# Optimization experiments

Measured on AMD Instinct MI355X. Metric: run time of the kernel, lower is better.

Reference implementation:

```python
import jax, jax.numpy as jnp
import numpy as np

PATCH = 16
LOSS_WEIGHT = 1.0


def setup_inputs() -> dict:
    key = jax.random.key(0)
    cls_score = jax.random.normal(key, (8, 19, 512, 512), dtype=jnp.float32)
    return {"cls_score": cls_score}


def reference(cls_score):
    # Faithful to NuclearLoss(patch_size=16, use_softmax=True, inverse=False,
    # reduction='mean').
    N, C, H, W = cls_score.shape
    p = PATCH
    ph, pw = H // p, W // p
    logits = jax.nn.softmax(cls_score, axis=1)  # softmax over channel dim
    # patchify: (N,C,H,W) -> (N*L, p*p, C) with L = ph*pw
    x = logits.reshape(N, C, ph, p, pw, p)
    x = jnp.einsum('nchpwq->nhwpqc', x)
    patches = x.reshape(N * ph * pw, p * p, C)  # (B, p^2, C)
    # Original: mats = sqrt(bmm(P^T, P)) elementwise, loss = -sum(trace(mat)).
    # Only the diagonal of P^T P is needed: diag_k = sum_i P[i,k]^2.
    diag = jnp.sum(patches * patches, axis=1)          # (B, C)
    loss = -jnp.sum(jnp.sqrt(diag))
    loss = loss / patches.shape[0]                      # reduction='mean'
    return LOSS_WEIGHT * loss
```

## Files before the change

kernel.cpp:

```cpp
#include <hip/hip_runtime.h>
#include <math.h>


#define NIMG 8
#define CCH  19
#define HH   512
#define WW   512
#define CHST (HH * WW)

__global__ __launch_bounds__(256, 4) void nuclear_loss_kernel(
    const float* __restrict__ in, float* __restrict__ out) {
    __shared__ float psum[4 * CCH];

    const int tid = threadIdx.x;
    const int b   = blockIdx.x;
    const int n    = b >> 8;
    const int rem  = b & 255;
    const int prow = rem >> 3;
    const int creg = rem & 7;
    const int col  = (creg << 6) + (tid & 63);
    const int row0 = (prow << 4) + (tid >> 6);
    const int plocal = (tid & 63) >> 4;

    for (int i = tid; i < 4 * CCH; i += 256) psum[i] = 0.0f;
    __syncthreads();

    float part[CCH];
#pragma unroll
    for (int c = 0; c < CCH; ++c) part[c] = 0.0f;

    const float* base = in + (size_t)n * CCH * CHST + (size_t)row0 * WW + col;

#pragma unroll
    for (int i = 0; i < 4; ++i) {
        const float* p = base + (size_t)(i * 4) * WW;
        float e[CCH];
        float s = 0.0f;
#pragma unroll
        for (int c = 0; c < CCH; ++c) {
            e[c] = __expf(p[(size_t)c * CHST]);
            s += e[c];
        }
        const float inv = 1.0f / s;
#pragma unroll
        for (int c = 0; c < CCH; ++c) {
            const float t = e[c] * inv;
            part[c] = fmaf(t, t, part[c]);
        }
    }

#pragma unroll
    for (int c = 0; c < CCH; ++c) {
        float v = part[c];
        v += __shfl_down(v, 8, 16);
        v += __shfl_down(v, 4, 16);
        v += __shfl_down(v, 2, 16);
        v += __shfl_down(v, 1, 16);
        part[c] = v;
    }

    if ((tid & 15) == 0) {
#pragma unroll
        for (int c = 0; c < CCH; ++c)
            atomicAdd(&psum[plocal * CCH + c], part[c]);
    }
    __syncthreads();

    if (tid < 64) {
        float v = (tid < 4 * CCH) ? sqrtf(psum[tid]) : 0.0f;
        if (tid + 64 < 4 * CCH) v += sqrtf(psum[tid + 64]);
        v += __shfl_down(v, 32, 64);
        v += __shfl_down(v, 16, 64);
        v += __shfl_down(v, 8, 64);
        v += __shfl_down(v, 4, 64);
        v += __shfl_down(v, 2, 64);
        v += __shfl_down(v, 1, 64);
        if (tid == 0) atomicAdd(out, v * (-1.0f / 8192.0f));
    }
}

extern "C" void kernel_launch(void* const* d_in, const int* in_sizes, int n_in,
                              void* d_out, int out_size, void* d_ws, size_t ws_size,
                              hipStream_t stream) {
    const float* in = (const float*)d_in[0];
    float* out = (float*)d_out;
    hipMemsetAsync(out, 0, sizeof(float), stream);
    nuclear_loss_kernel<<<2048, 256, 0, stream>>>(in, out);
}
```

Measured before the change: 223.7 us.

## Stage image rows into LDS via global_load_lds and reduce patches through global atomics

The kernel now has one block per image row. It copies all 19 channels of the row into LDS with direct global-to-LDS 16-byte loads, and each thread then computes the softmax for two adjacent pixels. Per-patch channel sums are reduced across 8 lanes and accumulated into a workspace with global atomics. A second kernel takes the square roots and reduces to the scalar. The goal is wider, better-coalesced loads and more memory-level parallelism, at the cost of many more global atomics (16 rows contend per patch entry), an extra memset and an extra launch, plus about 38 KB of LDS per block, which limits occupancy.

```diff
diff --git a/kernel.cpp b/kernel.cpp
--- a/kernel.cpp
+++ b/kernel.cpp
@@ -2,80 +2,103 @@
 #include <math.h>
 
 
-#define NIMG 8
-#define CCH  19
-#define HH   512
-#define WW   512
-#define CHST (HH * WW)
+#define CCH   19
+#define WW    512
+#define CHST  (512 * 512)
+#define IMGST (CCH * CHST)
+#define NPATCH 8192
 
-__global__ __launch_bounds__(256, 4) void nuclear_loss_kernel(
-    const float* __restrict__ in, float* __restrict__ out) {
-    __shared__ float psum[4 * CCH];
+typedef float f2 __attribute__((ext_vector_type(2)));
 
-    const int tid = threadIdx.x;
-    const int b   = blockIdx.x;
-    const int n    = b >> 8;
-    const int rem  = b & 255;
-    const int prow = rem >> 3;
-    const int creg = rem & 7;
-    const int col  = (creg << 6) + (tid & 63);
-    const int row0 = (prow << 4) + (tid >> 6);
-    const int plocal = (tid & 63) >> 4;
+__global__ __launch_bounds__(256, 4) void nuclear_patch_kernel(
+    const float* __restrict__ in, float* __restrict__ ws) {
+    __shared__ float lds[CCH * WW];
 
-    for (int i = tid; i < 4 * CCH; i += 256) psum[i] = 0.0f;
+    const int tid  = threadIdx.x;
+    const int w    = tid >> 6;
+    const int lane = tid & 63;
+    const int b    = blockIdx.x;
+    const int n    = b >> 9;
+    const int row  = b & 511;
+
+    const float* grow = in + (size_t)n * IMGST + (size_t)row * WW;
+    for (int j = 0; j < 10; ++j) {
+        const int i = w + j * 4;
+        if (i < 2 * CCH) {
+            const int ch   = i >> 1;
+            const int half = i & 1;
+            const float* g = grow + (size_t)ch * CHST + half * 256 + lane * 4;
+            const float* l = &lds[ch * WW + half * 256];
+            __builtin_amdgcn_global_load_lds(
+                (const __attribute__((address_space(1))) unsigned int*)g,
+                (__attribute__((address_space(3))) unsigned int*)l,
+                16, 0, 0);
+        }
+    }
     __syncthreads();
+
+    const f2* ldsv = (const f2*)lds;
+    f2 e[CCH];
+    f2 s2 = {0.0f, 0.0f};
+#pragma unroll
+    for (int c = 0; c < CCH; ++c) {
+        f2 x = ldsv[c * 256 + tid];
+        f2 ev;
+        ev.x = __expf(x.x);
+        ev.y = __expf(x.y);
+        e[c] = ev;
+        s2 += ev;
+    }
+    const float ix = 1.0f / s2.x;
+    const float iy = 1.0f / s2.y;
 
     float part[CCH];
 #pragma unroll
-    for (int c = 0; c < CCH; ++c) part[c] = 0.0f;
-
-    const float* base = in + (size_t)n * CCH * CHST + (size_t)row0 * WW + col;
-
-#pragma unroll
-    for (int i = 0; i < 4; ++i) {
-        const float* p = base + (size_t)(i * 4) * WW;
-        float e[CCH];
-        float s = 0.0f;
-#pragma unroll
-        for (int c = 0; c < CCH; ++c) {
-            e[c] = __expf(p[(size_t)c * CHST]);
-            s += e[c];
-        }
-        const float inv = 1.0f / s;
-#pragma unroll
-        for (int c = 0; c < CCH; ++c) {
-            const float t = e[c] * inv;
-            part[c] = fmaf(t, t, part[c]);
-        }
+    for (int c = 0; c < CCH; ++c) {
+        const float px = e[c].x * ix;
+        const float py = e[c].y * iy;
+        part[c] = px * px + py * py;
     }
 
 #pragma unroll
     for (int c = 0; c < CCH; ++c) {
         float v = part[c];
-        v += __shfl_down(v, 8, 16);
-        v += __shfl_down(v, 4, 16);
-        v += __shfl_down(v, 2, 16);
-        v += __shfl_down(v, 1, 16);
+        v += __shfl_down(v, 4, 8);
+        v += __shfl_down(v, 2, 8);
+        v += __shfl_down(v, 1, 8);
         part[c] = v;
     }
 
-    if ((tid & 15) == 0) {
+    if ((lane & 7) == 0) {
+        const int pcol = tid >> 3;
+        const int pr   = row >> 4;
+        float* wsp = ws + ((size_t)((n * 32 + pr) * 32 + pcol)) * CCH;
 #pragma unroll
-        for (int c = 0; c < CCH; ++c)
-            atomicAdd(&psum[plocal * CCH + c], part[c]);
+        for (int c = 0; c < CCH; ++c) atomicAdd(&wsp[c], part[c]);
     }
+}
+
+__global__ __launch_bounds__(256) void nuclear_finish_kernel(
+    const float* __restrict__ ws, float* __restrict__ out) {
+    const int pid = blockIdx.x * 256 + threadIdx.x;
+    const float* p = ws + (size_t)pid * CCH;
+    float s = 0.0f;
+#pragma unroll
+    for (int c = 0; c < CCH; ++c) s += sqrtf(p[c]);
+
+    s += __shfl_down(s, 32, 64);
+    s += __shfl_down(s, 16, 64);
+    s += __shfl_down(s, 8, 64);
+    s += __shfl_down(s, 4, 64);
+    s += __shfl_down(s, 2, 64);
+    s += __shfl_down(s, 1, 64);
+
+    __shared__ float wsum[4];
+    if ((threadIdx.x & 63) == 0) wsum[threadIdx.x >> 6] = s;
     __syncthreads();
-
-    if (tid < 64) {
-        float v = (tid < 4 * CCH) ? sqrtf(psum[tid]) : 0.0f;
-        if (tid + 64 < 4 * CCH) v += sqrtf(psum[tid + 64]);
-        v += __shfl_down(v, 32, 64);
-        v += __shfl_down(v, 16, 64);
-        v += __shfl_down(v, 8, 64);
-        v += __shfl_down(v, 4, 64);
-        v += __shfl_down(v, 2, 64);
-        v += __shfl_down(v, 1, 64);
-        if (tid == 0) atomicAdd(out, v * (-1.0f / 8192.0f));
+    if (threadIdx.x == 0) {
+        const float t = wsum[0] + wsum[1] + wsum[2] + wsum[3];
+        atomicAdd(out, t * (-1.0f / 8192.0f));
     }
 }
 
@@ -83,7 +106,12 @@
                               void* d_out, int out_size, void* d_ws, size_t ws_size,
                               hipStream_t stream) {
     const float* in = (const float*)d_in[0];
+    float* ws  = (float*)d_ws;
     float* out = (float*)d_out;
+
+    hipMemsetAsync(ws, 0, (size_t)NPATCH * CCH * sizeof(float), stream);
     hipMemsetAsync(out, 0, sizeof(float), stream);
-    nuclear_loss_kernel<<<2048, 256, 0, stream>>>(in, out);
+
+    nuclear_patch_kernel<<<4096, 256, 0, stream>>>(in, ws);
+    nuclear_finish_kernel<<<NPATCH / 256, 256, 0, stream>>>(ws, out);
 }
```

Result: slower. 330.5 us (+47.8%).

## Process full patch-row slabs per block with vectorized two-pass softmax loads

Applied to the files above, without the earlier changes.

Each 1024-thread block now covers a 16-row slab (one patch row) of an image, and every thread handles 8 contiguous pixels through float4 loads. Softmax is computed in two passes, with the second pass re-reading the input from global memory, so HBM or cache traffic for the input roughly doubles. In exchange it avoids holding 19 exponentials per pixel in registers. Per-patch partials are reduced through plain LDS stores instead of shared-memory atomics, and only one global atomic is issued per block. The grid shrinks from 2048 to 256 blocks, which may underfill the GPU's many CUs.

```diff
diff --git a/kernel.cpp b/kernel.cpp
--- a/kernel.cpp
+++ b/kernel.cpp
@@ -2,80 +2,98 @@
 #include <math.h>
 
 
-#define NIMG 8
-#define CCH  19
-#define HH   512
-#define WW   512
-#define CHST (HH * WW)
+#define CCH   19
+#define CHST  (512 * 512)
+#define IMGST (CCH * CHST)
 
-__global__ __launch_bounds__(256, 4) void nuclear_loss_kernel(
+typedef float f4 __attribute__((ext_vector_type(4)));
+
+__global__ __launch_bounds__(1024, 4) void nuclear_slab_kernel(
     const float* __restrict__ in, float* __restrict__ out) {
-    __shared__ float psum[4 * CCH];
+    __shared__ float psum[16 * 32 * CCH];
+    __shared__ float wsum[16];
 
-    const int tid = threadIdx.x;
-    const int b   = blockIdx.x;
-    const int n    = b >> 8;
-    const int rem  = b & 255;
-    const int prow = rem >> 3;
-    const int creg = rem & 7;
-    const int col  = (creg << 6) + (tid & 63);
-    const int row0 = (prow << 4) + (tid >> 6);
-    const int plocal = (tid & 63) >> 4;
+    const int tid  = threadIdx.x;
+    const int w    = tid >> 6;
+    const int lane = tid & 63;
+    const int b    = blockIdx.x;
+    const int n    = b >> 5;
+    const int prow = b & 31;
 
-    for (int i = tid; i < 4 * CCH; i += 256) psum[i] = 0.0f;
-    __syncthreads();
+    const float* base = in + (size_t)n * IMGST + (size_t)prow * 8192
+                           + (size_t)tid * 8;
+
+    f4 sA = {0.0f, 0.0f, 0.0f, 0.0f};
+    f4 sB = {0.0f, 0.0f, 0.0f, 0.0f};
+#pragma unroll
+    for (int c = 0; c < CCH; ++c) {
+        const f4* p = (const f4*)(base + (size_t)c * CHST);
+        const f4 xa = p[0];
+        const f4 xb = p[1];
+        f4 ea, eb;
+        ea.x = __expf(xa.x); ea.y = __expf(xa.y);
+        ea.z = __expf(xa.z); ea.w = __expf(xa.w);
+        eb.x = __expf(xb.x); eb.y = __expf(xb.y);
+        eb.z = __expf(xb.z); eb.w = __expf(xb.w);
+        sA += ea;
+        sB += eb;
+    }
+    f4 iA, iB;
+    iA.x = 1.0f / sA.x; iA.y = 1.0f / sA.y;
+    iA.z = 1.0f / sA.z; iA.w = 1.0f / sA.w;
+    iB.x = 1.0f / sB.x; iB.y = 1.0f / sB.y;
+    iB.z = 1.0f / sB.z; iB.w = 1.0f / sB.w;
 
     float part[CCH];
 #pragma unroll
     for (int c = 0; c < CCH; ++c) part[c] = 0.0f;
 
-    const float* base = in + (size_t)n * CCH * CHST + (size_t)row0 * WW + col;
-
 #pragma unroll
-    for (int i = 0; i < 4; ++i) {
-        const float* p = base + (size_t)(i * 4) * WW;
-        float e[CCH];
-        float s = 0.0f;
-#pragma unroll
-        for (int c = 0; c < CCH; ++c) {
-            e[c] = __expf(p[(size_t)c * CHST]);
-            s += e[c];
-        }
-        const float inv = 1.0f / s;
-#pragma unroll
-        for (int c = 0; c < CCH; ++c) {
-            const float t = e[c] * inv;
-            part[c] = fmaf(t, t, part[c]);
-        }
+    for (int c = 0; c < CCH; ++c) {
+        const f4* p = (const f4*)(base + (size_t)c * CHST);
+        const f4 xa = p[0];
+        const f4 xb = p[1];
+        f4 ea, eb;
+        ea.x = __expf(xa.x); ea.y = __expf(xa.y);
+        ea.z = __expf(xa.z); ea.w = __expf(xa.w);
+        eb.x = __expf(xb.x); eb.y = __expf(xb.y);
+        eb.z = __expf(xb.z); eb.w = __expf(xb.w);
+        const f4 pa = ea * iA;
+        const f4 pb = eb * iB;
+        float v = pa.x * pa.x + pa.y * pa.y + pa.z * pa.z + pa.w * pa.w
+                + pb.x * pb.x + pb.y * pb.y + pb.z * pb.z + pb.w * pb.w;
+        v += __shfl_down(v, 1, 2);
+        part[c] += v;
     }
 
+    if ((lane & 1) == 0) {
+        const int pc = lane >> 1;
+        float* dst = &psum[(w * 32 + pc) * CCH];
 #pragma unroll
-    for (int c = 0; c < CCH; ++c) {
-        float v = part[c];
-        v += __shfl_down(v, 8, 16);
-        v += __shfl_down(v, 4, 16);
-        v += __shfl_down(v, 2, 16);
-        v += __shfl_down(v, 1, 16);
-        part[c] = v;
-    }
-
-    if ((tid & 15) == 0) {
-#pragma unroll
-        for (int c = 0; c < CCH; ++c)
-            atomicAdd(&psum[plocal * CCH + c], part[c]);
+        for (int c = 0; c < CCH; ++c) dst[c] = part[c];
     }
     __syncthreads();
 
-    if (tid < 64) {
-        float v = (tid < 4 * CCH) ? sqrtf(psum[tid]) : 0.0f;
-        if (tid + 64 < 4 * CCH) v += sqrtf(psum[tid + 64]);
-        v += __shfl_down(v, 32, 64);
-        v += __shfl_down(v, 16, 64);
-        v += __shfl_down(v, 8, 64);
-        v += __shfl_down(v, 4, 64);
-        v += __shfl_down(v, 2, 64);
-        v += __shfl_down(v, 1, 64);
-        if (tid == 0) atomicAdd(out, v * (-1.0f / 8192.0f));
+    float v = 0.0f;
+    if (tid < 32 * CCH) {
+        float d = 0.0f;
+#pragma unroll
+        for (int r = 0; r < 16; ++r) d += psum[r * (32 * CCH) + tid];
+        v = sqrtf(d);
+    }
+    v += __shfl_down(v, 32, 64);
+    v += __shfl_down(v, 16, 64);
+    v += __shfl_down(v, 8, 64);
+    v += __shfl_down(v, 4, 64);
+    v += __shfl_down(v, 2, 64);
+    v += __shfl_down(v, 1, 64);
+    if (lane == 0) wsum[w] = v;
+    __syncthreads();
+    if (tid == 0) {
+        float t = 0.0f;
+#pragma unroll
+        for (int r = 0; r < 16; ++r) t += wsum[r];
+        atomicAdd(out, t * (-1.0f / 8192.0f));
     }
 }
 
@@ -85,5 +103,5 @@
     const float* in = (const float*)d_in[0];
     float* out = (float*)d_out;
     hipMemsetAsync(out, 0, sizeof(float), stream);
-    nuclear_loss_kernel<<<2048, 256, 0, stream>>>(in, out);
+    nuclear_slab_kernel<<<256, 1024, 0, stream>>>(in, out);
 }
```

Result: slower. 255.1 us (+14.0%).
